# Kernel optimization log

Hardware: AMD Instinct MI355X
Metric: run time of the kernel (lower is better)

The kernel has to match this reference:

```python
import jax, jax.numpy as jnp
import numpy as np

B, C, H, W = 4, 512, 64, 64
R = 8
D = C // R  # inner channels = 64


def setup_inputs() -> dict:
    key = jax.random.key(0)
    k1, k2, k3 = jax.random.split(key, 3)
    x = jax.random.normal(k1, (B, C, H, W), dtype=jnp.float32)
    # 1x1 conv weights, stored as [out, in] (kernel spatial dims are 1)
    w_qkv = jax.random.normal(k2, (3 * D, C), dtype=jnp.float32) * (1.0 / np.sqrt(C))
    w_out = jax.random.normal(k3, (C, D), dtype=jnp.float32) * (1.0 / np.sqrt(D))
    # nn.Parameter(torch.zeros(1)) in the original; use nonzero so output != input
    scale = jnp.array([0.3], dtype=jnp.float32)
    return {"x": x, "w_qkv": w_qkv, "w_out": w_out, "scale": scale}


def reference(x, w_qkv, w_out, scale):
    b, c, h, w = x.shape
    hw = h * w
    # 1x1 conv == channel matmul
    t = jnp.einsum('oc,bchw->bohw', w_qkv, x)  # [B, 3D, H, W]
    d = t.shape[1] // 3
    key_ = t[:, :d].reshape(b, d, hw)      # chunk order: key, query, value
    query = t[:, d:2 * d].reshape(b, d, hw)
    value = t[:, 2 * d:].reshape(b, d, hw)
    # scores[b, k, q] = sum_d key[b,d,k] * query[b,d,q]
    scores = jnp.einsum('bdk,bdq->bkq', key_, query)  # [B, hw, hw]
    # NB: original uses Softmax(dim=1) -> normalize over the KEY axis
    attn = jax.nn.softmax(scores, axis=1)
    out = jnp.einsum('bdk,bkq->bdq', value, attn)     # [B, D, hw]
    out = out.reshape(b, d, h, w)
    out = jnp.einsum('oc,bchw->bohw', w_out, out)     # [B, C, H, W]
    return scale * out + x
```

## Files before the change

### kernel.cpp

```cpp
#include <hip/hip_runtime.h>
#include <hip/hip_bf16.h>
#include <string.h>

#define B_ 4
#define C_ 512
#define D_ 64
#define HW_ 4096
#define NCHUNK 4
#define KT_PER_CHUNK 16

typedef __attribute__((ext_vector_type(8))) short bf16x8;
typedef __attribute__((ext_vector_type(4))) float f32x4;

__device__ __forceinline__ unsigned short f2bf(float f) {
    unsigned int u = __builtin_bit_cast(unsigned int, f);
    u += 0x7fffu + ((u >> 16) & 1u);
    return (unsigned short)(u >> 16);
}

__device__ __forceinline__ unsigned int pack2bf(float lo, float hi) {
    __hip_bfloat162 h = __float22bfloat162_rn(float2{lo, hi});
    unsigned int r;
    memcpy(&r, &h, sizeof(r));
    return r;
}

#if __has_builtin(__builtin_amdgcn_exp2f)
#define EXP2(x) __builtin_amdgcn_exp2f(x)
#else
#define EXP2(x) __expf((x) * 0.6931471805599453f)
#endif

#define OFF_WQKV 0u
#define OFF_WOUT 196608u
#define OFF_PART 262144u
#define OFF_KT   17039360u
#define OFF_QT   19136512u
#define OFF_V    21233664u
#define OFF_ML   25427968u

__global__ __launch_bounds__(256) void k_convw(const float* __restrict__ wqkv,
                                               const float* __restrict__ wout,
                                               unsigned short* __restrict__ wq_b,
                                               unsigned short* __restrict__ wo_b) {
    int i = blockIdx.x * 256 + threadIdx.x;
    if (i < 192 * C_) wq_b[i] = f2bf(wqkv[i]);
    if (i < C_ * D_)  wo_b[i] = f2bf(wout[i]);
}

__global__ __launch_bounds__(256) void k_qkv(const float* __restrict__ x,
                                             const unsigned short* __restrict__ wq,
                                             unsigned short* __restrict__ kt,
                                             unsigned short* __restrict__ qt,
                                             unsigned short* __restrict__ v) {
    __shared__ float tile[64][33];
    __shared__ unsigned short xb[32][64];
    int pT = blockIdx.x, b = blockIdx.y;
    int tid = threadIdx.x, wid = tid >> 6, lane = tid & 63;
    int g = lane >> 4, r16 = lane & 15;
    int pp0 = pT * 32;
    int lp = tid & 31, lc = tid >> 5;
    int pl = tid >> 3, ch = tid & 7;

    float rx[8];
    auto gload = [&](int ct) {
        #pragma unroll
        for (int r = 0; r < 8; ++r)
            rx[r] = x[(size_t)(b * C_ + ct * 64 + lc * 8 + r) * HW_ + pp0 + lp];
    };

    f32x4 acc[3][2] = {};
    gload(0);
    for (int ct = 0; ct < 8; ++ct) {
        #pragma unroll
        for (int r = 0; r < 8; ++r) tile[lc * 8 + r][lp] = rx[r];
        __syncthreads();
        unsigned int pk[4];
        #pragma unroll
        for (int j = 0; j < 4; ++j)
            pk[j] = pack2bf(tile[ch * 8 + 2 * j][pl], tile[ch * 8 + 2 * j + 1][pl]);
        *(uint4*)(&xb[pl][0] + ((ch ^ (pl & 7)) << 3)) =
            make_uint4(pk[0], pk[1], pk[2], pk[3]);
        if (ct + 1 < 8) gload(ct + 1);
        __syncthreads();
        #pragma unroll
        for (int cs = 0; cs < 2; ++cs) {
            bf16x8 bb[2];
            #pragma unroll
            for (int ps = 0; ps < 2; ++ps) {
                int row = ps * 16 + r16;
                bb[ps] = *(const bf16x8*)(&xb[row][0] + (((cs * 4 + g) ^ (row & 7)) << 3));
            }
            #pragma unroll
            for (int ot = 0; ot < 3; ++ot) {
                bf16x8 a = *(const bf16x8*)(wq + (size_t)(wid * 48 + ot * 16 + r16) * C_
                                            + ct * 64 + cs * 32 + g * 8);
                #pragma unroll
                for (int ps = 0; ps < 2; ++ps)
                    acc[ot][ps] = __builtin_amdgcn_mfma_f32_16x16x32_bf16(a, bb[ps], acc[ot][ps], 0, 0, 0);
            }
        }
    }
    #pragma unroll
    for (int ot = 0; ot < 3; ++ot) {
        int obase = wid * 48 + ot * 16;
        int oT = obase >> 6;
        int dbase = (obase & 63) + 4 * g;
        #pragma unroll
        for (int ps = 0; ps < 2; ++ps) {
            int pp = pp0 + ps * 16 + r16;
            if (oT < 2) {
                unsigned short* dst = (oT == 0) ? kt : qt;
                float qs = (oT == 1) ? 1.4426950408889634f : 1.0f;
                unsigned int u0 = pack2bf(acc[ot][ps][0] * qs, acc[ot][ps][1] * qs);
                unsigned int u1 = pack2bf(acc[ot][ps][2] * qs, acc[ot][ps][3] * qs);
                *reinterpret_cast<uint2*>(dst + (size_t)(b * HW_ + pp) * D_ + dbase) =
                    make_uint2(u0, u1);
            } else {
                #pragma unroll
                for (int r = 0; r < 4; ++r)
                    v[(size_t)(b * D_ + dbase + r) * HW_ + pp] = f2bf(acc[ot][ps][r]);
            }
        }
    }
}

__global__ __launch_bounds__(256, 4) void k_attn(const unsigned short* __restrict__ kt,
                                                 const unsigned short* __restrict__ qt,
                                                 const unsigned short* __restrict__ v,
                                                 float* __restrict__ part,
                                                 float* __restrict__ ml) {
    __shared__ unsigned short klds[2][64][64];
    __shared__ unsigned short vlds[2][64][64];
    __shared__ unsigned short plds[4][16][64];
    int qT = blockIdx.x, chunk = blockIdx.y, b = blockIdx.z;
    int tid = threadIdx.x, wid = tid >> 6, lane = tid & 63;
    int g = lane >> 4, r16 = lane & 15;
    int q0 = qT * 64 + wid * 16;

    const unsigned short* qp = qt + (size_t)(b * HW_ + q0 + r16) * D_ + g * 8;
    bf16x8 qf0 = *(const bf16x8*)(qp);
    bf16x8 qf1 = *(const bf16x8*)(qp + 32);

    int isV = tid >> 7, tt = tid & 127;
    int srow = tt >> 1, shalf = tt & 1;
    const unsigned short* sbase = isV
        ? (v  + (size_t)b * D_ * HW_ + (size_t)srow * HW_ + shalf * 32)
        : (kt + (size_t)b * HW_ * D_ + (size_t)srow * D_  + shalf * 32);
    const int smul = isV ? 1 : D_;
    const int k0 = chunk * (KT_PER_CHUNK * 64);

    uint4 rr0, rr1, rr2, rr3;
    auto gload = [&](int t) {
        const uint4* s = (const uint4*)(sbase + (size_t)(k0 + t * 64) * smul);
        rr0 = s[0]; rr1 = s[1]; rr2 = s[2]; rr3 = s[3];
    };
    auto swrite = [&](int buf) {
        unsigned short* Lb = isV ? &vlds[buf][0][0] : &klds[buf][0][0];
        unsigned short* rowp = Lb + srow * 64;
        int swz = srow & 7, c0 = shalf * 4;
        *(uint4*)(rowp + (((c0 + 0) ^ swz) << 3)) = rr0;
        *(uint4*)(rowp + (((c0 + 1) ^ swz) << 3)) = rr1;
        *(uint4*)(rowp + (((c0 + 2) ^ swz) << 3)) = rr2;
        *(uint4*)(rowp + (((c0 + 3) ^ swz) << 3)) = rr3;
    };

    gload(0);
    swrite(0);
    gload(1);
    __syncthreads();

    f32x4 acc[4] = {};
    float lsum = 0.f;
    int cur = 0;
    unsigned short* pb = &plds[wid][0][0];

    for (int t = 0; t < KT_PER_CHUNK; ++t) {
        if (t + 1 < KT_PER_CHUNK) swrite(cur ^ 1);
        if (t + 2 < KT_PER_CHUNK) gload(t + 2);

        f32x4 s4v[4];
        #pragma unroll
        for (int ks = 0; ks < 4; ++ks) {
            int row = ks * 16 + r16;
            const unsigned short* rp = &klds[cur][0][0] + row * 64;
            int swz = row & 7;
            bf16x8 kf0 = *(const bf16x8*)(rp + ((g ^ swz) << 3));
            bf16x8 kf1 = *(const bf16x8*)(rp + (((g + 4) ^ swz) << 3));
            f32x4 z = {};
            z = __builtin_amdgcn_mfma_f32_16x16x32_bf16(kf0, qf0, z, 0, 0, 0);
            z = __builtin_amdgcn_mfma_f32_16x16x32_bf16(kf1, qf1, z, 0, 0, 0);
            s4v[ks] = z;
        }
        float tsum = 0.f;
        #pragma unroll
        for (int ks = 0; ks < 4; ++ks) {
            float e0 = EXP2(s4v[ks][0]);
            float e1 = EXP2(s4v[ks][1]);
            float e2 = EXP2(s4v[ks][2]);
            float e3 = EXP2(s4v[ks][3]);
            tsum += (e0 + e1) + (e2 + e3);
            unsigned int u0 = pack2bf(e0, e1);
            unsigned int u1 = pack2bf(e2, e3);
            int ch = (2 * ks + (g >> 1)) ^ (r16 & 7);
            *(uint2*)(pb + r16 * 64 + (ch << 3) + 4 * (g & 1)) = make_uint2(u0, u1);
        }
        lsum += tsum;
        asm volatile("s_waitcnt lgkmcnt(0)" ::: "memory");
        int pswz = r16 & 7;
        bf16x8 pf0 = *(const bf16x8*)(pb + r16 * 64 + ((g ^ pswz) << 3));
        bf16x8 pf1 = *(const bf16x8*)(pb + r16 * 64 + (((g + 4) ^ pswz) << 3));
        #pragma unroll
        for (int dt = 0; dt < 4; ++dt) {
            int row = dt * 16 + r16;
            const unsigned short* rp = &vlds[cur][0][0] + row * 64;
            int swz = row & 7;
            bf16x8 vf0 = *(const bf16x8*)(rp + ((g ^ swz) << 3));
            bf16x8 vf1 = *(const bf16x8*)(rp + (((g + 4) ^ swz) << 3));
            acc[dt] = __builtin_amdgcn_mfma_f32_16x16x32_bf16(vf0, pf0, acc[dt], 0, 0, 0);
            acc[dt] = __builtin_amdgcn_mfma_f32_16x16x32_bf16(vf1, pf1, acc[dt], 0, 0, 0);
        }
        __syncthreads();
        cur ^= 1;
    }

    lsum += __shfl_xor(lsum, 16);
    lsum += __shfl_xor(lsum, 32);

    int row = ((b * NCHUNK + chunk) * HW_) + q0 + r16;
    #pragma unroll
    for (int dt = 0; dt < 4; ++dt)
        *reinterpret_cast<f32x4*>(&part[(size_t)row * D_ + dt * 16 + 4 * g]) = acc[dt];
    if (g == 0) {
        ml[2 * row]     = 0.0f;
        ml[2 * row + 1] = lsum;
    }
}

__global__ __launch_bounds__(256) void k_out(const unsigned short* __restrict__ wo,
                                             const float* __restrict__ part,
                                             const float* __restrict__ ml,
                                             const float* __restrict__ x,
                                             const float* __restrict__ scale,
                                             float* __restrict__ out) {
    __shared__ unsigned short alds[32][64];
    int pT = blockIdx.x, b = blockIdx.y;
    int tid = threadIdx.x;
    int pp0 = pT * 32;
    {
        int pl = tid >> 3, dgg = tid & 7;
        int q = pp0 + pl;
        float wi[NCHUNK];
        {
            float mi[NCHUNK], li[NCHUNK];
            #pragma unroll
            for (int i = 0; i < NCHUNK; ++i) {
                int row = (b * NCHUNK + i) * HW_ + q;
                mi[i] = ml[2 * row];
                li[i] = ml[2 * row + 1];
            }
            float M = mi[0];
            #pragma unroll
            for (int i = 1; i < NCHUNK; ++i) M = fmaxf(M, mi[i]);
            float L = 0.f;
            #pragma unroll
            for (int i = 0; i < NCHUNK; ++i) {
                wi[i] = EXP2(mi[i] - M);
                L += wi[i] * li[i];
            }
            float invL = 1.0f / L;
            #pragma unroll
            for (int i = 0; i < NCHUNK; ++i) wi[i] *= invL;
        }
        float o8[8] = {};
        #pragma unroll
        for (int i = 0; i < NCHUNK; ++i) {
            const float* pvp = &part[(size_t)((b * NCHUNK + i) * HW_ + q) * D_ + dgg * 8];
            f32x4 pv0 = *(const f32x4*)(pvp);
            f32x4 pv1 = *(const f32x4*)(pvp + 4);
            o8[0] += wi[i] * pv0[0]; o8[1] += wi[i] * pv0[1];
            o8[2] += wi[i] * pv0[2]; o8[3] += wi[i] * pv0[3];
            o8[4] += wi[i] * pv1[0]; o8[5] += wi[i] * pv1[1];
            o8[6] += wi[i] * pv1[2]; o8[7] += wi[i] * pv1[3];
        }
        unsigned int pk[4];
        #pragma unroll
        for (int j = 0; j < 4; ++j)
            pk[j] = pack2bf(o8[2 * j], o8[2 * j + 1]);
        *(uint4*)(&alds[pl][0] + ((dgg ^ (pl & 7)) << 3)) =
            make_uint4(pk[0], pk[1], pk[2], pk[3]);
    }
    __syncthreads();
    int wid = tid >> 6, lane = tid & 63;
    int g = lane >> 4, r16 = lane & 15;
    float sc = scale[0];
    bf16x8 bfr[2][2];
    #pragma unroll
    for (int ps = 0; ps < 2; ++ps) {
        int row = ps * 16 + r16;
        const unsigned short* rp = &alds[row][0];
        int swz = row & 7;
        bfr[ps][0] = *(const bf16x8*)(rp + (((0 * 4 + g) ^ swz) << 3));
        bfr[ps][1] = *(const bf16x8*)(rp + (((1 * 4 + g) ^ swz) << 3));
    }
    #pragma unroll 2
    for (int ot = 0; ot < 8; ++ot) {
        int orow = wid * 128 + ot * 16;
        bf16x8 a0 = *(const bf16x8*)(wo + (size_t)(orow + r16) * D_ + g * 8);
        bf16x8 a1 = *(const bf16x8*)(wo + (size_t)(orow + r16) * D_ + 32 + g * 8);
        #pragma unroll
        for (int ps = 0; ps < 2; ++ps) {
            f32x4 acc = {};
            acc = __builtin_amdgcn_mfma_f32_16x16x32_bf16(a0, bfr[ps][0], acc, 0, 0, 0);
            acc = __builtin_amdgcn_mfma_f32_16x16x32_bf16(a1, bfr[ps][1], acc, 0, 0, 0);
            int o = orow + 4 * g;
            int pp = pp0 + ps * 16 + r16;
            size_t base = (size_t)(b * C_ + o) * HW_ + pp;
            #pragma unroll
            for (int r = 0; r < 4; ++r)
                out[base + (size_t)r * HW_] = sc * acc[r] + x[base + (size_t)r * HW_];
        }
    }
}

extern "C" void kernel_launch(void* const* d_in, const int* in_sizes, int n_in,
                              void* d_out, int out_size, void* d_ws, size_t ws_size,
                              hipStream_t stream) {
    const float* x     = (const float*)d_in[0];
    const float* wqkv  = (const float*)d_in[1];
    const float* wout  = (const float*)d_in[2];
    const float* scale = (const float*)d_in[3];
    char* ws = (char*)d_ws;
    unsigned short* wq_b = (unsigned short*)(ws + OFF_WQKV);
    unsigned short* wo_b = (unsigned short*)(ws + OFF_WOUT);
    float*          prt  = (float*)(ws + OFF_PART);
    unsigned short* ktb  = (unsigned short*)(ws + OFF_KT);
    unsigned short* qtb  = (unsigned short*)(ws + OFF_QT);
    unsigned short* vb   = (unsigned short*)(ws + OFF_V);
    float*          mlb  = (float*)(ws + OFF_ML);

    hipLaunchKernelGGL(k_convw, dim3(384), dim3(256), 0, stream, wqkv, wout, wq_b, wo_b);
    hipLaunchKernelGGL(k_qkv,   dim3(128, 4),   dim3(256), 0, stream, x, wq_b, ktb, qtb, vb);
    hipLaunchKernelGGL(k_attn,  dim3(64, NCHUNK, 4), dim3(256), 0, stream, ktb, qtb, vb, prt, mlb);
    hipLaunchKernelGGL(k_out,   dim3(128, 4),   dim3(256), 0, stream, wo_b, prt, mlb, x, scale,
                       (float*)d_out);
}
```

Before: 78.63 us.

## Process two query sub-tiles per wave in attention kernel to reuse K/V tiles

Result: faster. 76.86 us (-2.3%).

```diff
diff --git a/kernel.cpp b/kernel.cpp
--- a/kernel.cpp
+++ b/kernel.cpp
@@ -125,22 +125,25 @@
     }
 }
 
-__global__ __launch_bounds__(256, 4) void k_attn(const unsigned short* __restrict__ kt,
+__global__ __launch_bounds__(256, 2) void k_attn(const unsigned short* __restrict__ kt,
                                                  const unsigned short* __restrict__ qt,
                                                  const unsigned short* __restrict__ v,
                                                  float* __restrict__ part,
                                                  float* __restrict__ ml) {
     __shared__ unsigned short klds[2][64][64];
     __shared__ unsigned short vlds[2][64][64];
-    __shared__ unsigned short plds[4][16][64];
+    __shared__ unsigned short plds[4][32][64];
     int qT = blockIdx.x, chunk = blockIdx.y, b = blockIdx.z;
     int tid = threadIdx.x, wid = tid >> 6, lane = tid & 63;
     int g = lane >> 4, r16 = lane & 15;
-    int q0 = qT * 64 + wid * 16;
-
-    const unsigned short* qp = qt + (size_t)(b * HW_ + q0 + r16) * D_ + g * 8;
-    bf16x8 qf0 = *(const bf16x8*)(qp);
-    bf16x8 qf1 = *(const bf16x8*)(qp + 32);
+    int q0 = qT * 128 + wid * 32;
+
+    const unsigned short* qpA = qt + (size_t)(b * HW_ + q0 + r16) * D_ + g * 8;
+    const unsigned short* qpB = qpA + (size_t)16 * D_;
+    bf16x8 qf0A = *(const bf16x8*)(qpA);
+    bf16x8 qf1A = *(const bf16x8*)(qpA + 32);
+    bf16x8 qf0B = *(const bf16x8*)(qpB);
+    bf16x8 qf1B = *(const bf16x8*)(qpB + 32);
 
     int isV = tid >> 7, tt = tid & 127;
     int srow = tt >> 1, shalf = tt & 1;
@@ -170,8 +173,8 @@
     gload(1);
     __syncthreads();
 
-    f32x4 acc[4] = {};
-    float lsum = 0.f;
+    f32x4 accA[4] = {}, accB[4] = {};
+    float lsumA = 0.f, lsumB = 0.f;
     int cur = 0;
     unsigned short* pb = &plds[wid][0][0];
 
@@ -179,7 +182,7 @@
         if (t + 1 < KT_PER_CHUNK) swrite(cur ^ 1);
         if (t + 2 < KT_PER_CHUNK) gload(t + 2);
 
-        f32x4 s4v[4];
+        f32x4 sA[4], sB[4];
         #pragma unroll
         for (int ks = 0; ks < 4; ++ks) {
             int row = ks * 16 + r16;
@@ -187,29 +190,46 @@
             int swz = row & 7;
             bf16x8 kf0 = *(const bf16x8*)(rp + ((g ^ swz) << 3));
             bf16x8 kf1 = *(const bf16x8*)(rp + (((g + 4) ^ swz) << 3));
-            f32x4 z = {};
-            z = __builtin_amdgcn_mfma_f32_16x16x32_bf16(kf0, qf0, z, 0, 0, 0);
-            z = __builtin_amdgcn_mfma_f32_16x16x32_bf16(kf1, qf1, z, 0, 0, 0);
-            s4v[ks] = z;
-        }
-        float tsum = 0.f;
+            f32x4 za = {};
+            za = __builtin_amdgcn_mfma_f32_16x16x32_bf16(kf0, qf0A, za, 0, 0, 0);
+            za = __builtin_amdgcn_mfma_f32_16x16x32_bf16(kf1, qf1A, za, 0, 0, 0);
+            sA[ks] = za;
+            f32x4 zb = {};
+            zb = __builtin_amdgcn_mfma_f32_16x16x32_bf16(kf0, qf0B, zb, 0, 0, 0);
+            zb = __builtin_amdgcn_mfma_f32_16x16x32_bf16(kf1, qf1B, zb, 0, 0, 0);
+            sB[ks] = zb;
+        }
+        float tsA = 0.f, tsB = 0.f;
         #pragma unroll
         for (int ks = 0; ks < 4; ++ks) {
-            float e0 = EXP2(s4v[ks][0]);
-            float e1 = EXP2(s4v[ks][1]);
-            float e2 = EXP2(s4v[ks][2]);
-            float e3 = EXP2(s4v[ks][3]);
-            tsum += (e0 + e1) + (e2 + e3);
-            unsigned int u0 = pack2bf(e0, e1);
-            unsigned int u1 = pack2bf(e2, e3);
             int ch = (2 * ks + (g >> 1)) ^ (r16 & 7);
-            *(uint2*)(pb + r16 * 64 + (ch << 3) + 4 * (g & 1)) = make_uint2(u0, u1);
-        }
-        lsum += tsum;
+            {
+                float e0 = EXP2(sA[ks][0]);
+                float e1 = EXP2(sA[ks][1]);
+                float e2 = EXP2(sA[ks][2]);
+                float e3 = EXP2(sA[ks][3]);
+                tsA += (e0 + e1) + (e2 + e3);
+                *(uint2*)(pb + r16 * 64 + (ch << 3) + 4 * (g & 1)) =
+                    make_uint2(pack2bf(e0, e1), pack2bf(e2, e3));
+            }
+            {
+                float e0 = EXP2(sB[ks][0]);
+                float e1 = EXP2(sB[ks][1]);
+                float e2 = EXP2(sB[ks][2]);
+                float e3 = EXP2(sB[ks][3]);
+                tsB += (e0 + e1) + (e2 + e3);
+                *(uint2*)(pb + (r16 + 16) * 64 + (ch << 3) + 4 * (g & 1)) =
+                    make_uint2(pack2bf(e0, e1), pack2bf(e2, e3));
+            }
+        }
+        lsumA += tsA;
+        lsumB += tsB;
         asm volatile("s_waitcnt lgkmcnt(0)" ::: "memory");
         int pswz = r16 & 7;
-        bf16x8 pf0 = *(const bf16x8*)(pb + r16 * 64 + ((g ^ pswz) << 3));
-        bf16x8 pf1 = *(const bf16x8*)(pb + r16 * 64 + (((g + 4) ^ pswz) << 3));
+        bf16x8 pf0A = *(const bf16x8*)(pb + r16 * 64 + ((g ^ pswz) << 3));
+        bf16x8 pf1A = *(const bf16x8*)(pb + r16 * 64 + (((g + 4) ^ pswz) << 3));
+        bf16x8 pf0B = *(const bf16x8*)(pb + (r16 + 16) * 64 + ((g ^ pswz) << 3));
+        bf16x8 pf1B = *(const bf16x8*)(pb + (r16 + 16) * 64 + (((g + 4) ^ pswz) << 3));
         #pragma unroll
         for (int dt = 0; dt < 4; ++dt) {
             int row = dt * 16 + r16;
@@ -217,23 +237,32 @@
             int swz = row & 7;
             bf16x8 vf0 = *(const bf16x8*)(rp + ((g ^ swz) << 3));
             bf16x8 vf1 = *(const bf16x8*)(rp + (((g + 4) ^ swz) << 3));
-            acc[dt] = __builtin_amdgcn_mfma_f32_16x16x32_bf16(vf0, pf0, acc[dt], 0, 0, 0);
-            acc[dt] = __builtin_amdgcn_mfma_f32_16x16x32_bf16(vf1, pf1, acc[dt], 0, 0, 0);
+            accA[dt] = __builtin_amdgcn_mfma_f32_16x16x32_bf16(vf0, pf0A, accA[dt], 0, 0, 0);
+            accA[dt] = __builtin_amdgcn_mfma_f32_16x16x32_bf16(vf1, pf1A, accA[dt], 0, 0, 0);
+            accB[dt] = __builtin_amdgcn_mfma_f32_16x16x32_bf16(vf0, pf0B, accB[dt], 0, 0, 0);
+            accB[dt] = __builtin_amdgcn_mfma_f32_16x16x32_bf16(vf1, pf1B, accB[dt], 0, 0, 0);
         }
         __syncthreads();
         cur ^= 1;
     }
 
-    lsum += __shfl_xor(lsum, 16);
-    lsum += __shfl_xor(lsum, 32);
-
-    int row = ((b * NCHUNK + chunk) * HW_) + q0 + r16;
+    lsumA += __shfl_xor(lsumA, 16);
+    lsumA += __shfl_xor(lsumA, 32);
+    lsumB += __shfl_xor(lsumB, 16);
+    lsumB += __shfl_xor(lsumB, 32);
+
+    int rowA = ((b * NCHUNK + chunk) * HW_) + q0 + r16;
+    int rowB = rowA + 16;
     #pragma unroll
-    for (int dt = 0; dt < 4; ++dt)
-        *reinterpret_cast<f32x4*>(&part[(size_t)row * D_ + dt * 16 + 4 * g]) = acc[dt];
+    for (int dt = 0; dt < 4; ++dt) {
+        *reinterpret_cast<f32x4*>(&part[(size_t)rowA * D_ + dt * 16 + 4 * g]) = accA[dt];
+        *reinterpret_cast<f32x4*>(&part[(size_t)rowB * D_ + dt * 16 + 4 * g]) = accB[dt];
+    }
     if (g == 0) {
-        ml[2 * row]     = 0.0f;
-        ml[2 * row + 1] = lsum;
+        ml[2 * rowA]     = 0.0f;
+        ml[2 * rowA + 1] = lsumA;
+        ml[2 * rowB]     = 0.0f;
+        ml[2 * rowB + 1] = lsumB;
     }
 }
 
@@ -341,7 +370,7 @@
 
     hipLaunchKernelGGL(k_convw, dim3(384), dim3(256), 0, stream, wqkv, wout, wq_b, wo_b);
     hipLaunchKernelGGL(k_qkv,   dim3(128, 4),   dim3(256), 0, stream, x, wq_b, ktb, qtb, vb);
-    hipLaunchKernelGGL(k_attn,  dim3(64, NCHUNK, 4), dim3(256), 0, stream, ktb, qtb, vb, prt, mlb);
+    hipLaunchKernelGGL(k_attn,  dim3(32, NCHUNK, 4), dim3(256), 0, stream, ktb, qtb, vb, prt, mlb);
     hipLaunchKernelGGL(k_out,   dim3(128, 4),   dim3(256), 0, stream, wo_b, prt, mlb, x, scale,
                        (float*)d_out);
 }
```
